# Performance work log

Measured on AMD Instinct MI355X. Metric: run time of the kernel, lower is better.

## Reference

```python
import jax, jax.numpy as jnp
import numpy as np

# Module hyperparameters (from init_kwargs)
DEPTH = 4
SMOOTH_STEP_PARAM = 1.0
TREES_NUM = 16
INPUT_DIM = 2048
OUTPUT_DIM = 512
BATCH = 8192
NUM_LEAVES = 2 ** DEPTH          # 16
NUM_INTERNAL = NUM_LEAVES - 1    # 15


def _routing_matrix():
    """R[n, l] = +1 if leaf l is in the left subtree of node n (gate = s),
    -1 if in the right subtree (gate = 1 - s), 0 if node n not on leaf l's path.
    Node indexing: root = 0, children of n are 2n+1 (left), 2n+2 (right)."""
    R = np.zeros((NUM_INTERNAL, NUM_LEAVES), dtype=np.float32)
    for l in range(NUM_LEAVES):
        node = 0
        for lvl in range(DEPTH):
            bit = (l >> (DEPTH - 1 - lvl)) & 1  # 0 = go left, 1 = go right
            R[node, l] = 1.0 if bit == 0 else -1.0
            node = 2 * node + 1 + bit
    return R

ROUTE = jnp.asarray(_routing_matrix())  # [NUM_INTERNAL, NUM_LEAVES]


def smooth_step(v):
    # TEL smooth-step: t = clip(ssp * v + 0.5, 0, 1); s = -2t^3 + 3t^2
    t = jnp.clip(SMOOTH_STEP_PARAM * v + 0.5, 0.0, 1.0)
    return t * t * (3.0 - 2.0 * t)


def setup_inputs() -> dict:
    key = jax.random.key(0)
    k1, k2, k3 = jax.random.split(key, 3)
    x = jax.random.normal(k1, (BATCH, INPUT_DIM), dtype=jnp.float32)
    node_weights = jax.random.normal(k2, (TREES_NUM, INPUT_DIM, NUM_INTERNAL), dtype=jnp.float32) * 0.02
    leaf_weights = jax.random.normal(k3, (TREES_NUM, OUTPUT_DIM, NUM_LEAVES), dtype=jnp.float32) * 0.02
    return {"x": x, "node_weights": node_weights, "leaf_weights": leaf_weights}


def reference(x, node_weights, leaf_weights):
    # Node pre-activations for all trees: [B, T, NUM_INTERNAL]
    a = jnp.einsum('bi,tin->btn', x, node_weights)
    s = smooth_step(a)  # probability of routing LEFT at each internal node
    left = (ROUTE == 1.0)
    right = (ROUTE == -1.0)
    # Per-(node, leaf) routing factor; nodes off the path contribute 1.
    terms = jnp.where(left, s[..., None], jnp.where(right, 1.0 - s[..., None], 1.0))  # [B,T,NI,NL]
    leaf_prob = jnp.prod(terms, axis=2)  # [B, T, NUM_LEAVES]
    # Weighted leaf aggregation, summed over trees (sum_outputs=True)
    out = jnp.einsum('btl,tol->bo', leaf_prob, leaf_weights)  # [B, OUTPUT_DIM]
    return out
```

## Files before the change

kernel.cpp:

```cpp
#include <hip/hip_runtime.h>
#include <cstdint>
#include <cstddef>

typedef __fp16 half8 __attribute__((ext_vector_type(8)));
typedef float  f32x4 __attribute__((ext_vector_type(4)));

#define BATCH 8192
#define INDIM 2048
#define OUTD  512
#define NC    256
#define BM    32
#define BK    256
#define NCH   (INDIM / BK)

__device__ __forceinline__ half8 cvt8(float4 a, float4 b) {
  half8 h;
  h[0] = (__fp16)a.x; h[1] = (__fp16)a.y; h[2] = (__fp16)a.z; h[3] = (__fp16)a.w;
  h[4] = (__fp16)b.x; h[5] = (__fp16)b.y; h[6] = (__fp16)b.z; h[7] = (__fp16)b.w;
  return h;
}

__global__ __launch_bounds__(256)
void kprepW(const float* __restrict__ nw, __fp16* __restrict__ WrT) {
  __shared__ float Ls[128][16];
  const int tid = threadIdx.x;
  const int t  = blockIdx.x >> 4;
  const int k0 = (blockIdx.x & 15) * 128;
  const float* base = nw + ((size_t)t * INDIM + k0) * 15;
  #pragma unroll
  for (int i = 0; i < 8; i++) {
    int fl = tid + 256 * i;
    if (fl < 1920) {
      float v = base[fl];
      int kk = (int)(((unsigned)fl * 8739u) >> 17);
      int n  = fl - 15 * kk;
      Ls[kk][n] = v;
    }
  }
  __syncthreads();
  const int n  = tid >> 4;
  const int kc = tid & 15;
  half8 h = {};
  if (n < 15) {
    #pragma unroll
    for (int j = 0; j < 8; j++) h[j] = (__fp16)Ls[kc * 8 + j][n];
  }
  *(half8*)(WrT + (size_t)(16 * t + n) * INDIM + k0 + kc * 8) = h;
}

__global__ __launch_bounds__(256)
void kprepL(const float* __restrict__ lw, __fp16* __restrict__ LWrT) {
  __shared__ float Ls[128][17];
  const int tid = threadIdx.x;
  const int t  = blockIdx.x >> 2;
  const int o0 = (blockIdx.x & 3) * 128;
  const float* base = lw + ((size_t)t * OUTD + o0) * 16;
  #pragma unroll
  for (int i = 0; i < 8; i++) {
    int fl = tid + 256 * i;
    Ls[fl >> 4][fl & 15] = base[fl];
  }
  __syncthreads();
  const int ol = tid >> 1;
  const int h  = tid & 1;
  half8 v;
  #pragma unroll
  for (int j = 0; j < 8; j++) v[j] = (__fp16)Ls[ol][8 * h + j];
  *(half8*)(LWrT + (size_t)(o0 + ol) * NC + 16 * t + 8 * h) = v;
}

__global__ __launch_bounds__(512, 1)
void kfused(const float* __restrict__ x, const __fp16* __restrict__ WrT,
            const __fp16* __restrict__ LWrT, float* __restrict__ out) {
  __shared__ char   uni[BM * NC * 4];
  __shared__ __fp16 Ps[BM * NC];
  __fp16* Xs = (__fp16*)uni;
  float*  As = (float*)uni;

  const int tid  = threadIdx.x;
  const int lane = tid & 63;
  const int wv   = tid >> 6;
  const int l15  = lane & 15;
  const int lg   = lane >> 4;
  const int r0   = blockIdx.x * BM;
  const int sr   = tid >> 4;
  const int seg  = tid & 15;

  const float*  xrow  = x + (size_t)(r0 + sr) * INDIM + seg * 16;
  const __fp16* wbase = WrT + (size_t)(32 * wv + l15) * INDIM + lg * 8;

  const int sE0 = (sr * BK + seg * 16)     ^ ((sr & 7) << 3);
  const int sE1 = (sr * BK + seg * 16 + 8) ^ ((sr & 7) << 3);

  f32x4 acc1[2][2] = {};
  float4 px[4];

  {
    const float* p = xrow;
    float4 a0 = *(const float4*)(p);      float4 a1 = *(const float4*)(p + 4);
    float4 a2 = *(const float4*)(p + 8);  float4 a3 = *(const float4*)(p + 12);
    *(half8*)&Xs[sE0] = cvt8(a0, a1);
    *(half8*)&Xs[sE1] = cvt8(a2, a3);
  }
  __syncthreads();

  #pragma unroll 1
  for (int ch = 0; ch < NCH; ++ch) {
    const int cur = ch & 1;
    const bool more = (ch + 1 < NCH);
    if (more) {
      const float* p = xrow + (ch + 1) * BK;
      px[0] = *(const float4*)(p);      px[1] = *(const float4*)(p + 4);
      px[2] = *(const float4*)(p + 8);  px[3] = *(const float4*)(p + 12);
    }
    #pragma unroll
    for (int ks = 0; ks < BK / 32; ks++) {
      half8 bf0 = *(const half8*)(wbase + (size_t)0  * INDIM + ch * BK + ks * 32);
      half8 bf1 = *(const half8*)(wbase + (size_t)16 * INDIM + ch * BK + ks * 32);
      half8 af[2];
      #pragma unroll
      for (int mt = 0; mt < 2; mt++) {
        const int r = l15 + 16 * mt;
        const int e = (r * BK + ks * 32 + lg * 8) ^ ((r & 7) << 3);
        af[mt] = *(const half8*)&Xs[cur * (BM * BK) + e];
      }
      acc1[0][0] = __builtin_amdgcn_mfma_f32_16x16x32_f16(af[0], bf0, acc1[0][0], 0, 0, 0);
      acc1[0][1] = __builtin_amdgcn_mfma_f32_16x16x32_f16(af[0], bf1, acc1[0][1], 0, 0, 0);
      acc1[1][0] = __builtin_amdgcn_mfma_f32_16x16x32_f16(af[1], bf0, acc1[1][0], 0, 0, 0);
      acc1[1][1] = __builtin_amdgcn_mfma_f32_16x16x32_f16(af[1], bf1, acc1[1][1], 0, 0, 0);
    }
    if (more) {
      const int off = (cur ^ 1) * (BM * BK);
      *(half8*)&Xs[off + sE0] = cvt8(px[0], px[1]);
      *(half8*)&Xs[off + sE1] = cvt8(px[2], px[3]);
    }
    __syncthreads();
  }

  #pragma unroll
  for (int mt = 0; mt < 2; mt++)
    #pragma unroll
    for (int nt = 0; nt < 2; nt++)
      #pragma unroll
      for (int i = 0; i < 4; i++)
        As[(16 * mt + 4 * lg + i) * NC + 32 * wv + 16 * nt + l15] = acc1[mt][nt][i];
  __syncthreads();

  {
    const int row = tid >> 4, tr = tid & 15;
    float av[16];
    #pragma unroll
    for (int q = 0; q < 4; q++) {
      f32x4 v = *(const f32x4*)&As[row * NC + tr * 16 + 4 * q];
      av[4 * q + 0] = v[0]; av[4 * q + 1] = v[1];
      av[4 * q + 2] = v[2]; av[4 * q + 3] = v[3];
    }
    float sg[15];
    #pragma unroll
    for (int m = 0; m < 15; m++) {
      float t = fminf(fmaxf(av[m] + 0.5f, 0.f), 1.f);
      sg[m] = t * t * (3.f - 2.f * t);
    }
    float p[16];
    #pragma unroll
    for (int l = 0; l < 16; l++) {
      float pr = 1.f; int node = 0;
      #pragma unroll
      for (int L = 0; L < 4; L++) {
        int bit = (l >> (3 - L)) & 1;
        pr *= bit ? (1.f - sg[node]) : sg[node];
        node = 2 * node + 1 + bit;
      }
      p[l] = pr;
    }
    half8 h0, h1;
    #pragma unroll
    for (int j = 0; j < 8; j++) { h0[j] = (__fp16)p[j]; h1[j] = (__fp16)p[8 + j]; }
    const int base = row * NC + tr * 16;
    const int swz  = (row & 7) << 3;
    *(half8*)&Ps[(base) ^ swz]     = h0;
    *(half8*)&Ps[(base + 8) ^ swz] = h1;
  }
  __syncthreads();

  f32x4 acc2[2][4] = {};
  const __fp16* lbase = LWrT + (size_t)(64 * wv + l15) * NC + lg * 8;
  #pragma unroll
  for (int kc = 0; kc < 2; kc++) {
    half8 bf2[4][4];
    #pragma unroll
    for (int nt = 0; nt < 4; nt++)
      #pragma unroll
      for (int ks = 0; ks < 4; ks++)
        bf2[nt][ks] = *(const half8*)(lbase + (size_t)nt * 16 * NC + kc * 128 + ks * 32);
    #pragma unroll
    for (int ks = 0; ks < 4; ks++) {
      half8 af[2];
      #pragma unroll
      for (int mt = 0; mt < 2; mt++) {
        const int r = l15 + 16 * mt;
        const int e = (r * NC + kc * 128 + ks * 32 + lg * 8) ^ ((r & 7) << 3);
        af[mt] = *(const half8*)&Ps[e];
      }
      #pragma unroll
      for (int mt = 0; mt < 2; mt++)
        #pragma unroll
        for (int nt = 0; nt < 4; nt++)
          acc2[mt][nt] = __builtin_amdgcn_mfma_f32_16x16x32_f16(af[mt], bf2[nt][ks], acc2[mt][nt], 0, 0, 0);
    }
  }
  #pragma unroll
  for (int mt = 0; mt < 2; mt++)
    #pragma unroll
    for (int nt = 0; nt < 4; nt++)
      #pragma unroll
      for (int i = 0; i < 4; i++)
        out[(size_t)(r0 + 16 * mt + 4 * lg + i) * OUTD + 64 * wv + 16 * nt + l15] = acc2[mt][nt][i];
}

extern "C" void kernel_launch(void* const* d_in, const int* in_sizes, int n_in,
                              void* d_out, int out_size, void* d_ws, size_t ws_size,
                              hipStream_t stream) {
  const float* x  = (const float*)d_in[0];
  const float* nw = (const float*)d_in[1];
  const float* lw = (const float*)d_in[2];
  float* out = (float*)d_out;

  __fp16* WrT  = (__fp16*)d_ws;
  __fp16* LWrT = (__fp16*)((char*)d_ws + (size_t)NC * INDIM * 2);

  hipLaunchKernelGGL(kprepW, dim3(256), dim3(256), 0, stream, nw, WrT);
  hipLaunchKernelGGL(kprepL, dim3(64),  dim3(256), 0, stream, lw, LWrT);
  hipLaunchKernelGGL(kfused, dim3(BATCH / BM), dim3(512), 0, stream, x, WrT, LWrT, out);
}
```

Baseline: 146.7 us.

## Load x fragments directly from global into MFMA registers, drop LDS staging

The first GEMM no longer stages x through double-buffered shared memory with per-chunk barriers. Each wave now loads its own fp32 x fragments straight from global memory, converts them to fp16 in registers, and feeds them to MFMA in an unrolled loop with no syncs. This removes LDS traffic and barrier stalls. The cost is that all 8 waves redundantly load the same 32x2048 x tile, giving 8x the global/L2 read traffic for x, with uncoalesced 32-byte strided accesses.

```diff
diff --git a/kernel.cpp b/kernel.cpp
--- a/kernel.cpp
+++ b/kernel.cpp
@@ -10,8 +10,6 @@
 #define OUTD  512
 #define NC    256
 #define BM    32
-#define BK    256
-#define NCH   (INDIM / BK)
 
 __device__ __forceinline__ half8 cvt8(float4 a, float4 b) {
   half8 h;
@@ -72,10 +70,8 @@
 __global__ __launch_bounds__(512, 1)
 void kfused(const float* __restrict__ x, const __fp16* __restrict__ WrT,
             const __fp16* __restrict__ LWrT, float* __restrict__ out) {
-  __shared__ char   uni[BM * NC * 4];
+  __shared__ float  As[BM * NC];
   __shared__ __fp16 Ps[BM * NC];
-  __fp16* Xs = (__fp16*)uni;
-  float*  As = (float*)uni;
 
   const int tid  = threadIdx.x;
   const int lane = tid & 63;
@@ -83,58 +79,28 @@
   const int l15  = lane & 15;
   const int lg   = lane >> 4;
   const int r0   = blockIdx.x * BM;
-  const int sr   = tid >> 4;
-  const int seg  = tid & 15;
-
-  const float*  xrow  = x + (size_t)(r0 + sr) * INDIM + seg * 16;
-  const __fp16* wbase = WrT + (size_t)(32 * wv + l15) * INDIM + lg * 8;
-
-  const int sE0 = (sr * BK + seg * 16)     ^ ((sr & 7) << 3);
-  const int sE1 = (sr * BK + seg * 16 + 8) ^ ((sr & 7) << 3);
+
+  const float*  xr0 = x + (size_t)(r0 + l15) * INDIM + lg * 8;
+  const float*  xr1 = xr0 + (size_t)16 * INDIM;
+  const __fp16* wb0 = WrT + (size_t)(32 * wv + l15) * INDIM + lg * 8;
+  const __fp16* wb1 = wb0 + (size_t)16 * INDIM;
 
   f32x4 acc1[2][2] = {};
-  float4 px[4];
-
-  {
-    const float* p = xrow;
-    float4 a0 = *(const float4*)(p);      float4 a1 = *(const float4*)(p + 4);
-    float4 a2 = *(const float4*)(p + 8);  float4 a3 = *(const float4*)(p + 12);
-    *(half8*)&Xs[sE0] = cvt8(a0, a1);
-    *(half8*)&Xs[sE1] = cvt8(a2, a3);
-  }
-  __syncthreads();
-
-  #pragma unroll 1
-  for (int ch = 0; ch < NCH; ++ch) {
-    const int cur = ch & 1;
-    const bool more = (ch + 1 < NCH);
-    if (more) {
-      const float* p = xrow + (ch + 1) * BK;
-      px[0] = *(const float4*)(p);      px[1] = *(const float4*)(p + 4);
-      px[2] = *(const float4*)(p + 8);  px[3] = *(const float4*)(p + 12);
-    }
-    #pragma unroll
-    for (int ks = 0; ks < BK / 32; ks++) {
-      half8 bf0 = *(const half8*)(wbase + (size_t)0  * INDIM + ch * BK + ks * 32);
-      half8 bf1 = *(const half8*)(wbase + (size_t)16 * INDIM + ch * BK + ks * 32);
-      half8 af[2];
-      #pragma unroll
-      for (int mt = 0; mt < 2; mt++) {
-        const int r = l15 + 16 * mt;
-        const int e = (r * BK + ks * 32 + lg * 8) ^ ((r & 7) << 3);
-        af[mt] = *(const half8*)&Xs[cur * (BM * BK) + e];
-      }
-      acc1[0][0] = __builtin_amdgcn_mfma_f32_16x16x32_f16(af[0], bf0, acc1[0][0], 0, 0, 0);
-      acc1[0][1] = __builtin_amdgcn_mfma_f32_16x16x32_f16(af[0], bf1, acc1[0][1], 0, 0, 0);
-      acc1[1][0] = __builtin_amdgcn_mfma_f32_16x16x32_f16(af[1], bf0, acc1[1][0], 0, 0, 0);
-      acc1[1][1] = __builtin_amdgcn_mfma_f32_16x16x32_f16(af[1], bf1, acc1[1][1], 0, 0, 0);
-    }
-    if (more) {
-      const int off = (cur ^ 1) * (BM * BK);
-      *(half8*)&Xs[off + sE0] = cvt8(px[0], px[1]);
-      *(half8*)&Xs[off + sE1] = cvt8(px[2], px[3]);
-    }
-    __syncthreads();
+
+  #pragma unroll 8
+  for (int k0 = 0; k0 < INDIM; k0 += 32) {
+    float4 a0 = *(const float4*)(xr0 + k0);
+    float4 a1 = *(const float4*)(xr0 + k0 + 4);
+    float4 b0 = *(const float4*)(xr1 + k0);
+    float4 b1 = *(const float4*)(xr1 + k0 + 4);
+    half8  bf0 = *(const half8*)(wb0 + k0);
+    half8  bf1 = *(const half8*)(wb1 + k0);
+    half8  af0 = cvt8(a0, a1);
+    half8  af1 = cvt8(b0, b1);
+    acc1[0][0] = __builtin_amdgcn_mfma_f32_16x16x32_f16(af0, bf0, acc1[0][0], 0, 0, 0);
+    acc1[0][1] = __builtin_amdgcn_mfma_f32_16x16x32_f16(af0, bf1, acc1[0][1], 0, 0, 0);
+    acc1[1][0] = __builtin_amdgcn_mfma_f32_16x16x32_f16(af1, bf0, acc1[1][0], 0, 0, 0);
+    acc1[1][1] = __builtin_amdgcn_mfma_f32_16x16x32_f16(af1, bf1, acc1[1][1], 0, 0, 0);
   }
 
   #pragma unroll
```

Result: slower. 187.1 us (+27.5%).
